# Optimization experiments

Measured on AMD Instinct MI355X. Metric: run time of the kernel, lower is better.

Reference implementation:

```python
import jax, jax.numpy as jnp
import numpy as np

N = 40000   # nodes
E = 600000  # edges
F = 128     # feature/hidden dim
G = 64      # graphs in batch


def setup_inputs() -> dict:
    key = jax.random.key(0)
    ks = jax.random.split(key, 16)
    x = jax.random.normal(ks[0], (N, F), dtype=jnp.float32)
    src = jax.random.randint(ks[1], (E,), 0, N)
    dst = jax.random.randint(ks[2], (E,), 0, N)
    edge_index = jnp.stack([src, dst]).astype(jnp.int64)
    batch = jnp.sort(jax.random.randint(ks[3], (N,), 0, G)).astype(jnp.int64)
    s = 1.0 / np.sqrt(F)
    W0 = jax.random.normal(ks[4], (F, F), dtype=jnp.float32) * s
    b0 = jnp.zeros((F,), dtype=jnp.float32)
    W1 = jax.random.normal(ks[5], (F, F), dtype=jnp.float32) * s
    b1 = jnp.zeros((F,), dtype=jnp.float32)
    W2 = jax.random.normal(ks[6], (F, F), dtype=jnp.float32) * s
    b2 = jnp.zeros((F,), dtype=jnp.float32)
    lin_w = jax.random.normal(ks[7], (F, 1), dtype=jnp.float32) * s
    lin_b = jnp.zeros((1,), dtype=jnp.float32)
    return {"x": x, "edge_index": edge_index, "batch": batch,
            "W0": W0, "b0": b0, "W1": W1, "b1": b1, "W2": W2, "b2": b2,
            "lin_w": lin_w, "lin_b": lin_b}


def _gcn_conv(x, W, b, src, dst, norm, num_nodes):
    # PyG GCNConv: linear transform, gather source, normalize, scatter-add to dst, add bias
    h = x @ W                                  # [N, F_out]
    msg = h[src] * norm[:, None]               # [E+N, F_out]
    agg = jax.ops.segment_sum(msg, dst, num_segments=num_nodes)
    return agg + b


def reference(x, edge_index, batch, W0, b0, W1, b1, W2, b2, lin_w, lin_b):
    num_nodes = x.shape[0]
    loops = jnp.arange(num_nodes, dtype=edge_index.dtype)
    src = jnp.concatenate([edge_index[0], loops])   # add self-loops
    dst = jnp.concatenate([edge_index[1], loops])
    # symmetric normalization deg^-1/2 (degree over in-edges incl. self loops)
    deg = jax.ops.segment_sum(jnp.ones_like(src, dtype=x.dtype), dst,
                              num_segments=num_nodes)
    dinv = jnp.where(deg > 0, jax.lax.rsqrt(jnp.maximum(deg, 1e-12)), 0.0)
    norm = dinv[src] * dinv[dst]                    # [E+N]

    h = jax.nn.relu(_gcn_conv(x, W0, b0, src, dst, norm, num_nodes))
    h = jax.nn.relu(_gcn_conv(h, W1, b1, src, dst, norm, num_nodes))
    h = jax.nn.relu(_gcn_conv(h, W2, b2, src, dst, norm, num_nodes))

    # global_mean_pool over ragged graph segments
    sums = jax.ops.segment_sum(h, batch, num_segments=G)            # [G, F]
    counts = jax.ops.segment_sum(jnp.ones((num_nodes,), h.dtype), batch,
                                 num_segments=G)                    # [G]
    pooled = sums / jnp.maximum(counts, 1.0)[:, None]
    return pooled @ lin_w + lin_b                                   # [G, 1]
```

## Files before the change

### kernel.cpp

```cpp
#include <hip/hip_runtime.h>
#include <hip/hip_bf16.h>

#define F_DIM 128
#define POOL_SEG 16

typedef __attribute__((ext_vector_type(8))) short short8v;
typedef __attribute__((ext_vector_type(4))) float float4v;


__device__ __forceinline__ ushort f2bf(float f) {
    uint u = __float_as_uint(f);
    u += 0x7fffu + ((u >> 16) & 1u);
    return (ushort)(u >> 16);
}
__device__ __forceinline__ float bf2f(ushort h) {
    return __uint_as_float(((uint)h) << 16);
}
__device__ __forceinline__ void bf2x(uint u, float& a, float& b) {
    a = __uint_as_float((u & 0x0000ffffu) << 16);
    b = __uint_as_float(u & 0xffff0000u);
}


__global__ void count_kernel(const int* __restrict__ dst, int* __restrict__ deg, int E_) {
    int i = blockIdx.x * blockDim.x + threadIdx.x;
    if (i < E_) atomicAdd(&deg[dst[i]], 1);
}

__global__ void scan_blocksums_kernel(const int* __restrict__ deg, int* __restrict__ bsum, int N_) {
    __shared__ int s[256];
    int i = blockIdx.x * 256 + threadIdx.x;
    s[threadIdx.x] = (i < N_) ? deg[i] : 0;
    __syncthreads();
    for (int off = 128; off; off >>= 1) {
        if (threadIdx.x < off) s[threadIdx.x] += s[threadIdx.x + off];
        __syncthreads();
    }
    if (threadIdx.x == 0) bsum[blockIdx.x] = s[0];
}

__global__ void scan_final_kernel(const int* __restrict__ deg, const int* __restrict__ bsum,
                                  int* __restrict__ row_ptr, int* __restrict__ rfill,
                                  float* __restrict__ dinv, int N_, int E_) {
    __shared__ int s[256];
    __shared__ int sred[256];
    const int t = threadIdx.x;
    const int bid = blockIdx.x;
    const int i = bid * 256 + t;

    int pv = 0;
    for (int j = t; j < bid; j += 256) pv += bsum[j];
    sred[t] = pv;
    __syncthreads();
    for (int off = 128; off; off >>= 1) {
        if (t < off) sred[t] += sred[t + off];
        __syncthreads();
    }
    const int bpre = sred[0];

    int orig = (i < N_) ? deg[i] : 0;
    s[t] = orig;
    __syncthreads();
    for (int off = 1; off < 256; off <<= 1) {
        int v = (t >= off) ? s[t - off] : 0;
        __syncthreads();
        s[t] += v;
        __syncthreads();
    }
    int excl = s[t] - orig + bpre;
    if (i < N_) {
        row_ptr[i] = excl;
        rfill[i] = excl;
        dinv[i] = 1.0f / sqrtf((float)(orig + 1));
    }
    if (i == N_ - 1) row_ptr[N_] = E_;
}

__global__ void fill_kernel(const int* __restrict__ src, const int* __restrict__ dst,
                            int* __restrict__ cur, int* __restrict__ col_src, int E_) {
    int i = blockIdx.x * blockDim.x + threadIdx.x;
    if (i < E_) {
        int p = atomicAdd(&cur[dst[i]], 1);
        col_src[p] = src[i];
    }
}


__global__ __launch_bounds__(256) void prep_kernel(
    const float* __restrict__ W0, const float* __restrict__ W1, const float* __restrict__ W2,
    ushort* __restrict__ Wth, ushort* __restrict__ Wtl, int* __restrict__ deg, int N_)
{
    if (blockIdx.x >= 48) {
        int i = (blockIdx.x - 48) * 256 + threadIdx.x;
        if (i < N_) deg[i] = 0;
        return;
    }
    int layer = blockIdx.x >> 4;
    int chunkc = blockIdx.x & 15;
    const float* W = (layer == 0) ? W0 : (layer == 1) ? W1 : W2;
    int t = threadIdx.x;
    int c  = chunkc * 8 + (t >> 5);
    int k0 = (t & 31) * 4;
    ushort4 hi, lo;
    float v0 = W[(size_t)(k0 + 0) * F_DIM + c];
    float v1 = W[(size_t)(k0 + 1) * F_DIM + c];
    float v2 = W[(size_t)(k0 + 2) * F_DIM + c];
    float v3 = W[(size_t)(k0 + 3) * F_DIM + c];
    hi.x = f2bf(v0); lo.x = f2bf(v0 - bf2f(hi.x));
    hi.y = f2bf(v1); lo.y = f2bf(v1 - bf2f(hi.y));
    hi.z = f2bf(v2); lo.z = f2bf(v2 - bf2f(hi.z));
    hi.w = f2bf(v3); lo.w = f2bf(v3 - bf2f(hi.w));
    size_t o = (size_t)layer * F_DIM * F_DIM + (size_t)c * F_DIM + k0;
    *reinterpret_cast<ushort4*>(&Wth[o]) = hi;
    *reinterpret_cast<ushort4*>(&Wtl[o]) = lo;
}


__global__ __launch_bounds__(256) void gemm_scale_kernel(
    const float* __restrict__ in, const ushort* __restrict__ Wth, const ushort* __restrict__ Wtl,
    const float* __restrict__ dinv, ushort* __restrict__ outbf, int N_)
{
    __shared__ ushort Ah[64 * F_DIM];
    __shared__ ushort Al[64 * F_DIM];
    __shared__ ushort Bh[64 * F_DIM];
    __shared__ ushort Bl[64 * F_DIM];

    const int tid = threadIdx.x;
    const int brow = (blockIdx.x >> 1) * 64;
    const int bcol = (blockIdx.x & 1) * 64;

    #pragma unroll
    for (int i = 0; i < 4; ++i) {
        int chunk = tid + i * 256;
        int r  = chunk >> 4;
        int k0 = (chunk & 15) * 8;
        int row = brow + r;
        float f[8];
        if (row < N_) {
            float4 g0 = *reinterpret_cast<const float4*>(&in[(size_t)row * F_DIM + k0]);
            float4 g1 = *reinterpret_cast<const float4*>(&in[(size_t)row * F_DIM + k0 + 4]);
            f[0] = g0.x; f[1] = g0.y; f[2] = g0.z; f[3] = g0.w;
            f[4] = g1.x; f[5] = g1.y; f[6] = g1.z; f[7] = g1.w;
        } else {
            #pragma unroll
            for (int j = 0; j < 8; ++j) f[j] = 0.f;
        }
        ushort hi[8], lo[8];
        #pragma unroll
        for (int j = 0; j < 8; ++j) {
            hi[j] = f2bf(f[j]);
            lo[j] = f2bf(f[j] - bf2f(hi[j]));
        }
        int idx = r * F_DIM + (k0 ^ ((r & 7) << 3));
        *reinterpret_cast<short8v*>(&Ah[idx]) = *reinterpret_cast<short8v*>(hi);
        *reinterpret_cast<short8v*>(&Al[idx]) = *reinterpret_cast<short8v*>(lo);
    }
    #pragma unroll
    for (int i = 0; i < 4; ++i) {
        int chunk = tid + i * 256;
        int c  = chunk >> 4;
        int k0 = (chunk & 15) * 8;
        size_t go = (size_t)(bcol + c) * F_DIM + k0;
        int idx = c * F_DIM + (k0 ^ ((c & 7) << 3));
        *reinterpret_cast<short8v*>(&Bh[idx]) = *reinterpret_cast<const short8v*>(&Wth[go]);
        *reinterpret_cast<short8v*>(&Bl[idx]) = *reinterpret_cast<const short8v*>(&Wtl[go]);
    }
    __syncthreads();

    const int l = tid & 63;
    const int wave = tid >> 6;
    const int m0 = wave * 16;
    const int row_a = m0 + (l & 15);
    const int kgrp = (l >> 4) * 8;
    const int aswz = (row_a & 7) << 3;

    float4v acc[4] = {{0.f,0.f,0.f,0.f},{0.f,0.f,0.f,0.f},{0.f,0.f,0.f,0.f},{0.f,0.f,0.f,0.f}};

    #pragma unroll
    for (int kk = 0; kk < 4; ++kk) {
        int kbase = kk * 32 + kgrp;
        short8v a_h = *reinterpret_cast<short8v*>(&Ah[row_a * F_DIM + (kbase ^ aswz)]);
        short8v a_l = *reinterpret_cast<short8v*>(&Al[row_a * F_DIM + (kbase ^ aswz)]);
        #pragma unroll
        for (int n = 0; n < 4; ++n) {
            int col_b = n * 16 + (l & 15);
            int bidx = col_b * F_DIM + (kbase ^ ((col_b & 7) << 3));
            short8v b_h = *reinterpret_cast<short8v*>(&Bh[bidx]);
            short8v b_l = *reinterpret_cast<short8v*>(&Bl[bidx]);
            acc[n] = __builtin_amdgcn_mfma_f32_16x16x32_bf16(a_h, b_h, acc[n], 0, 0, 0);
            acc[n] = __builtin_amdgcn_mfma_f32_16x16x32_bf16(a_l, b_h, acc[n], 0, 0, 0);
            acc[n] = __builtin_amdgcn_mfma_f32_16x16x32_bf16(a_h, b_l, acc[n], 0, 0, 0);
        }
    }

    #pragma unroll
    for (int i = 0; i < 4; ++i) {
        int rloc = m0 + (l >> 4) * 4 + i;
        int row = brow + rloc;
        if (row < N_) {
            float s = dinv[row];
            #pragma unroll
            for (int n = 0; n < 4; ++n) {
                ushort o = f2bf(s * acc[n][i]);
                outbf[(size_t)row * F_DIM + bcol + n * 16 + (l & 15)] = o;
            }
        }
    }
}


__global__ __launch_bounds__(256) void gather_kernel(
    const ushort* __restrict__ Mbf, const int* __restrict__ row_ptr,
    const int* __restrict__ col_src, const float* __restrict__ dinv,
    const float* __restrict__ bias, float* __restrict__ Hout, int N_)
{
    int v = blockIdx.x * 4 + (threadIdx.x >> 6);
    if (v >= N_) return;
    const int lane = threadIdx.x & 63;
    const int fq  = lane & 15;
    const int sub = lane >> 4;
    const uint4* M4 = reinterpret_cast<const uint4*>(Mbf);

    float acc[8];
    #pragma unroll
    for (int j = 0; j < 8; ++j) acc[j] = 0.f;

    int lo = row_ptr[v];
    int total = row_ptr[v + 1] - lo + 1;

    for (int base = 0; base < total; base += 64) {
        int nidx = total - base; if (nidx > 64) nidx = 64;
        int p = base + lane;
        int idx = v;
        if (p > 0 && p < total) idx = col_src[lo + p - 1];

        int nslots = (nidx + 3) >> 2;
        int jfull  = (nidx >> 4) * 4;
        int j = 0;
        for (; j < jfull; j += 4) {
            int q0 = j * 4 + sub;
            int s0 = __shfl(idx, q0);
            int s1 = __shfl(idx, q0 + 4);
            int s2 = __shfl(idx, q0 + 8);
            int s3 = __shfl(idx, q0 + 12);
            uint4 u0 = M4[(size_t)s0 * 16 + fq];
            uint4 u1 = M4[(size_t)s1 * 16 + fq];
            uint4 u2 = M4[(size_t)s2 * 16 + fq];
            uint4 u3 = M4[(size_t)s3 * 16 + fq];
            float a, b;
            bf2x(u0.x, a, b); acc[0] += a; acc[1] += b;
            bf2x(u0.y, a, b); acc[2] += a; acc[3] += b;
            bf2x(u0.z, a, b); acc[4] += a; acc[5] += b;
            bf2x(u0.w, a, b); acc[6] += a; acc[7] += b;
            bf2x(u1.x, a, b); acc[0] += a; acc[1] += b;
            bf2x(u1.y, a, b); acc[2] += a; acc[3] += b;
            bf2x(u1.z, a, b); acc[4] += a; acc[5] += b;
            bf2x(u1.w, a, b); acc[6] += a; acc[7] += b;
            bf2x(u2.x, a, b); acc[0] += a; acc[1] += b;
            bf2x(u2.y, a, b); acc[2] += a; acc[3] += b;
            bf2x(u2.z, a, b); acc[4] += a; acc[5] += b;
            bf2x(u2.w, a, b); acc[6] += a; acc[7] += b;
            bf2x(u3.x, a, b); acc[0] += a; acc[1] += b;
            bf2x(u3.y, a, b); acc[2] += a; acc[3] += b;
            bf2x(u3.z, a, b); acc[4] += a; acc[5] += b;
            bf2x(u3.w, a, b); acc[6] += a; acc[7] += b;
        }
        if (j < nslots) {
            int q0 = j * 4 + sub;
            int q1 = q0 + 4, q2 = q0 + 8, q3 = q0 + 12;
            int c0 = min(q0, nidx - 1), c1 = min(q1, nidx - 1);
            int c2 = min(q2, nidx - 1), c3 = min(q3, nidx - 1);
            int s0 = __shfl(idx, c0);
            int s1 = __shfl(idx, c1);
            int s2 = __shfl(idx, c2);
            int s3 = __shfl(idx, c3);
            float m0 = (q0 < nidx) ? 1.f : 0.f;
            float m1 = (q1 < nidx) ? 1.f : 0.f;
            float m2 = (q2 < nidx) ? 1.f : 0.f;
            float m3 = (q3 < nidx) ? 1.f : 0.f;
            uint4 u0 = M4[(size_t)s0 * 16 + fq];
            uint4 u1 = M4[(size_t)s1 * 16 + fq];
            uint4 u2 = M4[(size_t)s2 * 16 + fq];
            uint4 u3 = M4[(size_t)s3 * 16 + fq];
            float a, b;
            bf2x(u0.x, a, b); acc[0] = fmaf(a, m0, acc[0]); acc[1] = fmaf(b, m0, acc[1]);
            bf2x(u0.y, a, b); acc[2] = fmaf(a, m0, acc[2]); acc[3] = fmaf(b, m0, acc[3]);
            bf2x(u0.z, a, b); acc[4] = fmaf(a, m0, acc[4]); acc[5] = fmaf(b, m0, acc[5]);
            bf2x(u0.w, a, b); acc[6] = fmaf(a, m0, acc[6]); acc[7] = fmaf(b, m0, acc[7]);
            bf2x(u1.x, a, b); acc[0] = fmaf(a, m1, acc[0]); acc[1] = fmaf(b, m1, acc[1]);
            bf2x(u1.y, a, b); acc[2] = fmaf(a, m1, acc[2]); acc[3] = fmaf(b, m1, acc[3]);
            bf2x(u1.z, a, b); acc[4] = fmaf(a, m1, acc[4]); acc[5] = fmaf(b, m1, acc[5]);
            bf2x(u1.w, a, b); acc[6] = fmaf(a, m1, acc[6]); acc[7] = fmaf(b, m1, acc[7]);
            bf2x(u2.x, a, b); acc[0] = fmaf(a, m2, acc[0]); acc[1] = fmaf(b, m2, acc[1]);
            bf2x(u2.y, a, b); acc[2] = fmaf(a, m2, acc[2]); acc[3] = fmaf(b, m2, acc[3]);
            bf2x(u2.z, a, b); acc[4] = fmaf(a, m2, acc[4]); acc[5] = fmaf(b, m2, acc[5]);
            bf2x(u2.w, a, b); acc[6] = fmaf(a, m2, acc[6]); acc[7] = fmaf(b, m2, acc[7]);
            bf2x(u3.x, a, b); acc[0] = fmaf(a, m3, acc[0]); acc[1] = fmaf(b, m3, acc[1]);
            bf2x(u3.y, a, b); acc[2] = fmaf(a, m3, acc[2]); acc[3] = fmaf(b, m3, acc[3]);
            bf2x(u3.z, a, b); acc[4] = fmaf(a, m3, acc[4]); acc[5] = fmaf(b, m3, acc[5]);
            bf2x(u3.w, a, b); acc[6] = fmaf(a, m3, acc[6]); acc[7] = fmaf(b, m3, acc[7]);
        }
    }

    #pragma unroll
    for (int j = 0; j < 8; ++j) {
        acc[j] += __shfl_xor(acc[j], 16);
        acc[j] += __shfl_xor(acc[j], 32);
    }

    if (sub == 0) {
        float dv = dinv[v];
        const float4* b4 = reinterpret_cast<const float4*>(bias);
        float4 bb0 = b4[fq * 2], bb1 = b4[fq * 2 + 1];
        float4 o0, o1;
        o0.x = fmaxf(dv * acc[0] + bb0.x, 0.0f);
        o0.y = fmaxf(dv * acc[1] + bb0.y, 0.0f);
        o0.z = fmaxf(dv * acc[2] + bb0.z, 0.0f);
        o0.w = fmaxf(dv * acc[3] + bb0.w, 0.0f);
        o1.x = fmaxf(dv * acc[4] + bb1.x, 0.0f);
        o1.y = fmaxf(dv * acc[5] + bb1.y, 0.0f);
        o1.z = fmaxf(dv * acc[6] + bb1.z, 0.0f);
        o1.w = fmaxf(dv * acc[7] + bb1.w, 0.0f);
        float4* H4 = reinterpret_cast<float4*>(&Hout[(size_t)v * F_DIM + fq * 8]);
        H4[0] = o0;
        H4[1] = o1;
    }
}


__device__ __forceinline__ int lower_bound_i(const int* __restrict__ a, int n, int key) {
    int lo = 0, hi = n;
    while (lo < hi) {
        int mid = (lo + hi) >> 1;
        if (a[mid] < key) lo = mid + 1; else hi = mid;
    }
    return lo;
}

__global__ __launch_bounds__(128) void pool_part_kernel(
    const float* __restrict__ H, const int* __restrict__ batch,
    float* __restrict__ partial, int N_)
{
    int g = blockIdx.x / POOL_SEG;
    int s = blockIdx.x % POOL_SEG;
    int lo = lower_bound_i(batch, N_, g);
    int hi = lower_bound_i(batch, N_, g + 1);
    int len = hi - lo;
    int chunk = (len + POOL_SEG - 1) / POOL_SEG;
    int a = lo + s * chunk;
    int b = min(a + chunk, hi);
    int col = threadIdx.x;
    float acc = 0.f;
    for (int n = a; n < b; ++n) acc += H[(size_t)n * F_DIM + col];
    partial[((size_t)g * POOL_SEG + s) * F_DIM + col] = acc;
}

__global__ __launch_bounds__(128) void pool_final_kernel(
    const float* __restrict__ partial, const int* __restrict__ batch,
    const float* __restrict__ lin_w, const float* __restrict__ lin_b,
    float* __restrict__ out, int N_)
{
    int g = blockIdx.x;
    int col = threadIdx.x;
    float acc = 0.f;
    #pragma unroll
    for (int s = 0; s < POOL_SEG; ++s)
        acc += partial[((size_t)g * POOL_SEG + s) * F_DIM + col];
    int lo = lower_bound_i(batch, N_, g);
    int hi = lower_bound_i(batch, N_, g + 1);
    float pooled = acc / fmaxf((float)(hi - lo), 1.0f);
    float v = pooled * lin_w[col];
    __shared__ float sm[128];
    sm[col] = v;
    __syncthreads();
    if (col < 64) {
        float t = sm[col] + sm[col + 64];
        for (int off = 32; off; off >>= 1) t += __shfl_down(t, off);
        if (col == 0) out[g] = t + lin_b[0];
    }
}


extern "C" void kernel_launch(void* const* d_in, const int* in_sizes, int n_in,
                              void* d_out, int out_size, void* d_ws, size_t ws_size,
                              hipStream_t stream) {
    const float* x     = (const float*)d_in[0];
    const int*   ei    = (const int*)d_in[1];
    const int*   batch = (const int*)d_in[2];
    const float* W0    = (const float*)d_in[3];
    const float* b0    = (const float*)d_in[4];
    const float* W1    = (const float*)d_in[5];
    const float* b1    = (const float*)d_in[6];
    const float* W2    = (const float*)d_in[7];
    const float* b2    = (const float*)d_in[8];
    const float* lin_w = (const float*)d_in[9];
    const float* lin_b = (const float*)d_in[10];

    const int N_ = in_sizes[2];
    const int E_ = in_sizes[1] / 2;
    const int G_ = out_size;
    const int* esrc = ei;
    const int* edst = ei + E_;

    char* p = reinterpret_cast<char*>(d_ws);
    ushort* Mbf = reinterpret_cast<ushort*>(p);        p += (size_t)N_ * F_DIM * sizeof(ushort);
    float*  Hbuf = reinterpret_cast<float*>(p);        p += (size_t)N_ * F_DIM * sizeof(float);
    float*  dinvp = reinterpret_cast<float*>(p);       p += (size_t)N_ * sizeof(float);
    int*    deg = reinterpret_cast<int*>(p);           p += (size_t)N_ * sizeof(int);
    int*    row_ptr = reinterpret_cast<int*>(p);       p += (size_t)(N_ + 4) * sizeof(int);
    int*    rfill = reinterpret_cast<int*>(p);         p += (size_t)N_ * sizeof(int);
    int*    col_src = reinterpret_cast<int*>(p);       p += (size_t)E_ * sizeof(int);
    ushort* Wth = reinterpret_cast<ushort*>(p);        p += (size_t)3 * F_DIM * F_DIM * sizeof(ushort);
    ushort* Wtl = reinterpret_cast<ushort*>(p);        p += (size_t)3 * F_DIM * F_DIM * sizeof(ushort);
    const int NB = (N_ + 255) / 256;
    int*    bsum = reinterpret_cast<int*>(p);          p += (size_t)NB * sizeof(int);
    float*  partial = reinterpret_cast<float*>(d_ws);

    int eb = (E_ + 255) / 256;
    prep_kernel<<<48 + NB, 256, 0, stream>>>(W0, W1, W2, Wth, Wtl, deg, N_);
    count_kernel<<<eb, 256, 0, stream>>>(edst, deg, E_);
    scan_blocksums_kernel<<<NB, 256, 0, stream>>>(deg, bsum, N_);
    scan_final_kernel<<<NB, 256, 0, stream>>>(deg, bsum, row_ptr, rfill, dinvp, N_, E_);
    fill_kernel<<<eb, 256, 0, stream>>>(esrc, edst, rfill, col_src, E_);

    const int gemm_grid = ((N_ + 63) / 64) * 2;
    const int gat_grid  = (N_ + 3) / 4;

    const float* cur_in = x;
    const float* bias[3] = {b0, b1, b2};
    for (int l = 0; l < 3; ++l) {
        gemm_scale_kernel<<<gemm_grid, 256, 0, stream>>>(
            cur_in, Wth + (size_t)l * F_DIM * F_DIM, Wtl + (size_t)l * F_DIM * F_DIM,
            dinvp, Mbf, N_);
        gather_kernel<<<gat_grid, 256, 0, stream>>>(
            Mbf, row_ptr, col_src, dinvp, bias[l], Hbuf, N_);
        cur_in = Hbuf;
    }

    pool_part_kernel<<<G_ * POOL_SEG, 128, 0, stream>>>(Hbuf, batch, partial, N_);
    pool_final_kernel<<<G_, 128, 0, stream>>>(partial, batch, lin_w, lin_b, (float*)d_out, N_);
}
```

Baseline: 214.7 us.

## Fuse CSR fill into first GEMM, drop blocksum scan, store hidden as bf16 hi/lo

The CSR fill pass now runs as extra blocks of the first-layer GEMM launch, and the separate block-sum kernel is removed because each scan block sums its own prefix of the degree array. The gather kernel writes its hidden output pre-split into bf16 hi/lo halves, so the next GEMM loads them directly and skips the fp32-to-bf16 split in its load phase. Together these cut kernel launches and per-layer conversion work. The cost is that scan blocks redundantly re-read the degree prefix (quadratic in block count), and pooling now reads two bf16 arrays.

```diff
diff --git a/kernel.cpp b/kernel.cpp
--- a/kernel.cpp
+++ b/kernel.cpp
@@ -19,70 +19,6 @@
 __device__ __forceinline__ void bf2x(uint u, float& a, float& b) {
     a = __uint_as_float((u & 0x0000ffffu) << 16);
     b = __uint_as_float(u & 0xffff0000u);
-}
-
-
-__global__ void count_kernel(const int* __restrict__ dst, int* __restrict__ deg, int E_) {
-    int i = blockIdx.x * blockDim.x + threadIdx.x;
-    if (i < E_) atomicAdd(&deg[dst[i]], 1);
-}
-
-__global__ void scan_blocksums_kernel(const int* __restrict__ deg, int* __restrict__ bsum, int N_) {
-    __shared__ int s[256];
-    int i = blockIdx.x * 256 + threadIdx.x;
-    s[threadIdx.x] = (i < N_) ? deg[i] : 0;
-    __syncthreads();
-    for (int off = 128; off; off >>= 1) {
-        if (threadIdx.x < off) s[threadIdx.x] += s[threadIdx.x + off];
-        __syncthreads();
-    }
-    if (threadIdx.x == 0) bsum[blockIdx.x] = s[0];
-}
-
-__global__ void scan_final_kernel(const int* __restrict__ deg, const int* __restrict__ bsum,
-                                  int* __restrict__ row_ptr, int* __restrict__ rfill,
-                                  float* __restrict__ dinv, int N_, int E_) {
-    __shared__ int s[256];
-    __shared__ int sred[256];
-    const int t = threadIdx.x;
-    const int bid = blockIdx.x;
-    const int i = bid * 256 + t;
-
-    int pv = 0;
-    for (int j = t; j < bid; j += 256) pv += bsum[j];
-    sred[t] = pv;
-    __syncthreads();
-    for (int off = 128; off; off >>= 1) {
-        if (t < off) sred[t] += sred[t + off];
-        __syncthreads();
-    }
-    const int bpre = sred[0];
-
-    int orig = (i < N_) ? deg[i] : 0;
-    s[t] = orig;
-    __syncthreads();
-    for (int off = 1; off < 256; off <<= 1) {
-        int v = (t >= off) ? s[t - off] : 0;
-        __syncthreads();
-        s[t] += v;
-        __syncthreads();
-    }
-    int excl = s[t] - orig + bpre;
-    if (i < N_) {
-        row_ptr[i] = excl;
-        rfill[i] = excl;
-        dinv[i] = 1.0f / sqrtf((float)(orig + 1));
-    }
-    if (i == N_ - 1) row_ptr[N_] = E_;
-}
-
-__global__ void fill_kernel(const int* __restrict__ src, const int* __restrict__ dst,
-                            int* __restrict__ cur, int* __restrict__ col_src, int E_) {
-    int i = blockIdx.x * blockDim.x + threadIdx.x;
-    if (i < E_) {
-        int p = atomicAdd(&cur[dst[i]], 1);
-        col_src[p] = src[i];
-    }
 }
 
 
@@ -116,14 +52,70 @@
 }
 
 
-__global__ __launch_bounds__(256) void gemm_scale_kernel(
+__global__ void count_kernel(const int* __restrict__ dst, int* __restrict__ deg, int E_) {
+    int i = blockIdx.x * blockDim.x + threadIdx.x;
+    if (i < E_) atomicAdd(&deg[dst[i]], 1);
+}
+
+__global__ void scan_final_kernel(const int* __restrict__ deg,
+                                  int* __restrict__ row_ptr, int* __restrict__ rfill,
+                                  float* __restrict__ dinv, int N_, int E_) {
+    __shared__ int s[256];
+    __shared__ int sred[256];
+    const int t = threadIdx.x;
+    const int bid = blockIdx.x;
+    const int i = bid * 256 + t;
+    const int pre_end = bid * 256;
+
+    int pv = 0;
+    for (int j = t; j < pre_end; j += 256) pv += deg[j];
+    sred[t] = pv;
+    __syncthreads();
+    for (int off = 128; off; off >>= 1) {
+        if (t < off) sred[t] += sred[t + off];
+        __syncthreads();
+    }
+    const int bpre = sred[0];
+
+    int orig = (i < N_) ? deg[i] : 0;
+    s[t] = orig;
+    __syncthreads();
+    for (int off = 1; off < 256; off <<= 1) {
+        int v = (t >= off) ? s[t - off] : 0;
+        __syncthreads();
+        s[t] += v;
+        __syncthreads();
+    }
+    int excl = s[t] - orig + bpre;
+    if (i < N_) {
+        row_ptr[i] = excl;
+        rfill[i] = excl;
+        dinv[i] = 1.0f / sqrtf((float)(orig + 1));
+    }
+    if (i == N_ - 1) row_ptr[N_] = E_;
+}
+
+
+__global__ __launch_bounds__(256) void gemm1_fill_kernel(
     const float* __restrict__ in, const ushort* __restrict__ Wth, const ushort* __restrict__ Wtl,
-    const float* __restrict__ dinv, ushort* __restrict__ outbf, int N_)
+    const float* __restrict__ dinv, ushort* __restrict__ outbf,
+    const int* __restrict__ esrc, const int* __restrict__ edst,
+    int* __restrict__ rfill, int* __restrict__ col_src,
+    int N_, int E_, int gemm_grid)
 {
     __shared__ ushort Ah[64 * F_DIM];
     __shared__ ushort Al[64 * F_DIM];
     __shared__ ushort Bh[64 * F_DIM];
     __shared__ ushort Bl[64 * F_DIM];
+
+    if ((int)blockIdx.x >= gemm_grid) {
+        int e = ((int)blockIdx.x - gemm_grid) * 256 + threadIdx.x;
+        if (e < E_) {
+            int p = atomicAdd(&rfill[edst[e]], 1);
+            col_src[p] = esrc[e];
+        }
+        return;
+    }
 
     const int tid = threadIdx.x;
     const int brow = (blockIdx.x >> 1) * 64;
@@ -209,10 +201,97 @@
 }
 
 
+__global__ __launch_bounds__(256) void gemm_bf_kernel(
+    const ushort* __restrict__ inh, const ushort* __restrict__ inl,
+    const ushort* __restrict__ Wth, const ushort* __restrict__ Wtl,
+    const float* __restrict__ dinv, ushort* __restrict__ outbf, int N_)
+{
+    __shared__ ushort Ah[64 * F_DIM];
+    __shared__ ushort Al[64 * F_DIM];
+    __shared__ ushort Bh[64 * F_DIM];
+    __shared__ ushort Bl[64 * F_DIM];
+
+    const int tid = threadIdx.x;
+    const int brow = (blockIdx.x >> 1) * 64;
+    const int bcol = (blockIdx.x & 1) * 64;
+
+    #pragma unroll
+    for (int i = 0; i < 4; ++i) {
+        int chunk = tid + i * 256;
+        int r  = chunk >> 4;
+        int k0 = (chunk & 15) * 8;
+        int row = brow + r;
+        short8v h, l;
+        if (row < N_) {
+            h = *reinterpret_cast<const short8v*>(&inh[(size_t)row * F_DIM + k0]);
+            l = *reinterpret_cast<const short8v*>(&inl[(size_t)row * F_DIM + k0]);
+        } else {
+            h = short8v{0,0,0,0,0,0,0,0};
+            l = short8v{0,0,0,0,0,0,0,0};
+        }
+        int idx = r * F_DIM + (k0 ^ ((r & 7) << 3));
+        *reinterpret_cast<short8v*>(&Ah[idx]) = h;
+        *reinterpret_cast<short8v*>(&Al[idx]) = l;
+    }
+    #pragma unroll
+    for (int i = 0; i < 4; ++i) {
+        int chunk = tid + i * 256;
+        int c  = chunk >> 4;
+        int k0 = (chunk & 15) * 8;
+        size_t go = (size_t)(bcol + c) * F_DIM + k0;
+        int idx = c * F_DIM + (k0 ^ ((c & 7) << 3));
+        *reinterpret_cast<short8v*>(&Bh[idx]) = *reinterpret_cast<const short8v*>(&Wth[go]);
+        *reinterpret_cast<short8v*>(&Bl[idx]) = *reinterpret_cast<const short8v*>(&Wtl[go]);
+    }
+    __syncthreads();
+
+    const int l = tid & 63;
+    const int wave = tid >> 6;
+    const int m0 = wave * 16;
+    const int row_a = m0 + (l & 15);
+    const int kgrp = (l >> 4) * 8;
+    const int aswz = (row_a & 7) << 3;
+
+    float4v acc[4] = {{0.f,0.f,0.f,0.f},{0.f,0.f,0.f,0.f},{0.f,0.f,0.f,0.f},{0.f,0.f,0.f,0.f}};
+
+    #pragma unroll
+    for (int kk = 0; kk < 4; ++kk) {
+        int kbase = kk * 32 + kgrp;
+        short8v a_h = *reinterpret_cast<short8v*>(&Ah[row_a * F_DIM + (kbase ^ aswz)]);
+        short8v a_l = *reinterpret_cast<short8v*>(&Al[row_a * F_DIM + (kbase ^ aswz)]);
+        #pragma unroll
+        for (int n = 0; n < 4; ++n) {
+            int col_b = n * 16 + (l & 15);
+            int bidx = col_b * F_DIM + (kbase ^ ((col_b & 7) << 3));
+            short8v b_h = *reinterpret_cast<short8v*>(&Bh[bidx]);
+            short8v b_l = *reinterpret_cast<short8v*>(&Bl[bidx]);
+            acc[n] = __builtin_amdgcn_mfma_f32_16x16x32_bf16(a_h, b_h, acc[n], 0, 0, 0);
+            acc[n] = __builtin_amdgcn_mfma_f32_16x16x32_bf16(a_l, b_h, acc[n], 0, 0, 0);
+            acc[n] = __builtin_amdgcn_mfma_f32_16x16x32_bf16(a_h, b_l, acc[n], 0, 0, 0);
+        }
+    }
+
+    #pragma unroll
+    for (int i = 0; i < 4; ++i) {
+        int rloc = m0 + (l >> 4) * 4 + i;
+        int row = brow + rloc;
+        if (row < N_) {
+            float s = dinv[row];
+            #pragma unroll
+            for (int n = 0; n < 4; ++n) {
+                ushort o = f2bf(s * acc[n][i]);
+                outbf[(size_t)row * F_DIM + bcol + n * 16 + (l & 15)] = o;
+            }
+        }
+    }
+}
+
+
 __global__ __launch_bounds__(256) void gather_kernel(
     const ushort* __restrict__ Mbf, const int* __restrict__ row_ptr,
     const int* __restrict__ col_src, const float* __restrict__ dinv,
-    const float* __restrict__ bias, float* __restrict__ Hout, int N_)
+    const float* __restrict__ bias,
+    ushort* __restrict__ Hh, ushort* __restrict__ Hl, int N_)
 {
     int v = blockIdx.x * 4 + (threadIdx.x >> 6);
     if (v >= N_) return;
@@ -312,18 +391,23 @@
         float dv = dinv[v];
         const float4* b4 = reinterpret_cast<const float4*>(bias);
         float4 bb0 = b4[fq * 2], bb1 = b4[fq * 2 + 1];
-        float4 o0, o1;
-        o0.x = fmaxf(dv * acc[0] + bb0.x, 0.0f);
-        o0.y = fmaxf(dv * acc[1] + bb0.y, 0.0f);
-        o0.z = fmaxf(dv * acc[2] + bb0.z, 0.0f);
-        o0.w = fmaxf(dv * acc[3] + bb0.w, 0.0f);
-        o1.x = fmaxf(dv * acc[4] + bb1.x, 0.0f);
-        o1.y = fmaxf(dv * acc[5] + bb1.y, 0.0f);
-        o1.z = fmaxf(dv * acc[6] + bb1.z, 0.0f);
-        o1.w = fmaxf(dv * acc[7] + bb1.w, 0.0f);
-        float4* H4 = reinterpret_cast<float4*>(&Hout[(size_t)v * F_DIM + fq * 8]);
-        H4[0] = o0;
-        H4[1] = o1;
+        float vals[8];
+        vals[0] = fmaxf(dv * acc[0] + bb0.x, 0.0f);
+        vals[1] = fmaxf(dv * acc[1] + bb0.y, 0.0f);
+        vals[2] = fmaxf(dv * acc[2] + bb0.z, 0.0f);
+        vals[3] = fmaxf(dv * acc[3] + bb0.w, 0.0f);
+        vals[4] = fmaxf(dv * acc[4] + bb1.x, 0.0f);
+        vals[5] = fmaxf(dv * acc[5] + bb1.y, 0.0f);
+        vals[6] = fmaxf(dv * acc[6] + bb1.z, 0.0f);
+        vals[7] = fmaxf(dv * acc[7] + bb1.w, 0.0f);
+        ushort hi8[8], lo8[8];
+        #pragma unroll
+        for (int j = 0; j < 8; ++j) {
+            hi8[j] = f2bf(vals[j]);
+            lo8[j] = f2bf(vals[j] - bf2f(hi8[j]));
+        }
+        *reinterpret_cast<uint4*>(&Hh[(size_t)v * F_DIM + fq * 8]) = *reinterpret_cast<uint4*>(hi8);
+        *reinterpret_cast<uint4*>(&Hl[(size_t)v * F_DIM + fq * 8]) = *reinterpret_cast<uint4*>(lo8);
     }
 }
 
@@ -338,8 +422,8 @@
 }
 
 __global__ __launch_bounds__(128) void pool_part_kernel(
-    const float* __restrict__ H, const int* __restrict__ batch,
-    float* __restrict__ partial, int N_)
+    const ushort* __restrict__ Hh, const ushort* __restrict__ Hl,
+    const int* __restrict__ batch, float* __restrict__ partial, int N_)
 {
     int g = blockIdx.x / POOL_SEG;
     int s = blockIdx.x % POOL_SEG;
@@ -351,7 +435,8 @@
     int b = min(a + chunk, hi);
     int col = threadIdx.x;
     float acc = 0.f;
-    for (int n = a; n < b; ++n) acc += H[(size_t)n * F_DIM + col];
+    for (int n = a; n < b; ++n)
+        acc += bf2f(Hh[(size_t)n * F_DIM + col]) + bf2f(Hl[(size_t)n * F_DIM + col]);
     partial[((size_t)g * POOL_SEG + s) * F_DIM + col] = acc;
 }
 
@@ -404,7 +489,8 @@
 
     char* p = reinterpret_cast<char*>(d_ws);
     ushort* Mbf = reinterpret_cast<ushort*>(p);        p += (size_t)N_ * F_DIM * sizeof(ushort);
-    float*  Hbuf = reinterpret_cast<float*>(p);        p += (size_t)N_ * F_DIM * sizeof(float);
+    ushort* Hh  = reinterpret_cast<ushort*>(p);        p += (size_t)N_ * F_DIM * sizeof(ushort);
+    ushort* Hl  = reinterpret_cast<ushort*>(p);        p += (size_t)N_ * F_DIM * sizeof(ushort);
     float*  dinvp = reinterpret_cast<float*>(p);       p += (size_t)N_ * sizeof(float);
     int*    deg = reinterpret_cast<int*>(p);           p += (size_t)N_ * sizeof(int);
     int*    row_ptr = reinterpret_cast<int*>(p);       p += (size_t)(N_ + 4) * sizeof(int);
@@ -412,31 +498,34 @@
     int*    col_src = reinterpret_cast<int*>(p);       p += (size_t)E_ * sizeof(int);
     ushort* Wth = reinterpret_cast<ushort*>(p);        p += (size_t)3 * F_DIM * F_DIM * sizeof(ushort);
     ushort* Wtl = reinterpret_cast<ushort*>(p);        p += (size_t)3 * F_DIM * F_DIM * sizeof(ushort);
+    float*  partial = reinterpret_cast<float*>(d_ws);
+
     const int NB = (N_ + 255) / 256;
-    int*    bsum = reinterpret_cast<int*>(p);          p += (size_t)NB * sizeof(int);
-    float*  partial = reinterpret_cast<float*>(d_ws);
-
-    int eb = (E_ + 255) / 256;
+    const int eb = (E_ + 255) / 256;
+    const int gemm_grid = ((N_ + 63) / 64) * 2;
+    const int gat_grid  = (N_ + 3) / 4;
+
     prep_kernel<<<48 + NB, 256, 0, stream>>>(W0, W1, W2, Wth, Wtl, deg, N_);
     count_kernel<<<eb, 256, 0, stream>>>(edst, deg, E_);
-    scan_blocksums_kernel<<<NB, 256, 0, stream>>>(deg, bsum, N_);
-    scan_final_kernel<<<NB, 256, 0, stream>>>(deg, bsum, row_ptr, rfill, dinvp, N_, E_);
-    fill_kernel<<<eb, 256, 0, stream>>>(esrc, edst, rfill, col_src, E_);
-
-    const int gemm_grid = ((N_ + 63) / 64) * 2;
-    const int gat_grid  = (N_ + 3) / 4;
-
-    const float* cur_in = x;
-    const float* bias[3] = {b0, b1, b2};
-    for (int l = 0; l < 3; ++l) {
-        gemm_scale_kernel<<<gemm_grid, 256, 0, stream>>>(
-            cur_in, Wth + (size_t)l * F_DIM * F_DIM, Wtl + (size_t)l * F_DIM * F_DIM,
-            dinvp, Mbf, N_);
-        gather_kernel<<<gat_grid, 256, 0, stream>>>(
-            Mbf, row_ptr, col_src, dinvp, bias[l], Hbuf, N_);
-        cur_in = Hbuf;
-    }
-
-    pool_part_kernel<<<G_ * POOL_SEG, 128, 0, stream>>>(Hbuf, batch, partial, N_);
+    scan_final_kernel<<<NB, 256, 0, stream>>>(deg, row_ptr, rfill, dinvp, N_, E_);
+
+    gemm1_fill_kernel<<<gemm_grid + eb, 256, 0, stream>>>(
+        x, Wth, Wtl, dinvp, Mbf, esrc, edst, rfill, col_src, N_, E_, gemm_grid);
+    gather_kernel<<<gat_grid, 256, 0, stream>>>(
+        Mbf, row_ptr, col_src, dinvp, b0, Hh, Hl, N_);
+
+    gemm_bf_kernel<<<gemm_grid, 256, 0, stream>>>(
+        Hh, Hl, Wth + (size_t)1 * F_DIM * F_DIM, Wtl + (size_t)1 * F_DIM * F_DIM,
+        dinvp, Mbf, N_);
+    gather_kernel<<<gat_grid, 256, 0, stream>>>(
+        Mbf, row_ptr, col_src, dinvp, b1, Hh, Hl, N_);
+
+    gemm_bf_kernel<<<gemm_grid, 256, 0, stream>>>(
+        Hh, Hl, Wth + (size_t)2 * F_DIM * F_DIM, Wtl + (size_t)2 * F_DIM * F_DIM,
+        dinvp, Mbf, N_);
+    gather_kernel<<<gat_grid, 256, 0, stream>>>(
+        Mbf, row_ptr, col_src, dinvp, b2, Hh, Hl, N_);
+
+    pool_part_kernel<<<G_ * POOL_SEG, 128, 0, stream>>>(Hh, Hl, batch, partial, N_);
     pool_final_kernel<<<G_, 128, 0, stream>>>(partial, batch, lin_w, lin_b, (float*)d_out, N_);
 }
```

Result: slower. 228.2 us (+6.3%).
